# Kernel optimization log

Hardware: AMD Instinct MI355X
Metric: run time of the kernel (lower is better)

Reference implementation:

```python
import jax, jax.numpy as jnp
import numpy as np

N_HEAD = 16
N_EMBD = 1024
HEAD_DIM = N_EMBD // N_HEAD


def setup_inputs() -> dict:
    key = jax.random.key(0)
    k1, k2, k3 = jax.random.split(key, 3)
    B, T, C = 2, 2048, N_EMBD
    x = jax.random.normal(k1, (B, T, C), dtype=jnp.float32)
    # nn.Linear weights: (out_features, in_features)
    W_attn = jax.random.normal(k2, (3 * C, C), dtype=jnp.float32) * 0.02
    W_proj = jax.random.normal(k3, (C, C), dtype=jnp.float32) * 0.02
    return {"x": x, "W_attn": W_attn, "W_proj": W_proj}


def reference(x, W_attn, W_proj):
    B, T, C = x.shape
    h, hd = N_HEAD, HEAD_DIM
    # c_attn: x @ W^T, then split into q, k, v
    qkv = jnp.einsum('btc,dc->btd', x, W_attn)  # [B, T, 3C]
    q, k, v = jnp.split(qkv, 3, axis=-1)
    # [B, T, C] -> [B, h, T, hd]
    q = q.reshape(B, T, h, hd).transpose(0, 2, 1, 3)
    k = k.reshape(B, T, h, hd).transpose(0, 2, 1, 3)
    v = v.reshape(B, T, h, hd).transpose(0, 2, 1, 3)
    # NOTE: no 1/sqrt(hd) scaling in the original module
    logits = jnp.einsum('bhnk,bhmk->bhnm', q, k)  # [B, h, T, T]
    causal = jnp.tril(jnp.ones((T, T), dtype=bool))  # [T, T]
    logits = jnp.where(causal[None, None, :, :], logits, -jnp.inf)
    weights = jax.nn.softmax(logits, axis=-1)
    O = jnp.einsum('bhnm,bhmv->bhnv', weights, v)  # [B, h, T, hd]
    # Original: einsum('bhnv,hdv->bnd', O, c_proj.weight) with weight viewed as (h, d, v)
    Wp = W_proj.reshape(h, C, hd)
    Y = jnp.einsum('bhnv,hdv->bnd', O, Wp)  # [B, T, C]
    return Y
```

## Files before the change

kernel.cpp:

```cpp
#include <hip/hip_runtime.h>
#include <stdint.h>
#include <math.h>

#define B_    2
#define T_    2048
#define C_    1024
#define H_    16
#define D_    64
#define MTOT  4096
#define NQKV  3072
#define KDIM  1024

#define LOG2E 1.4426950408889634f

typedef short short8 __attribute__((ext_vector_type(8)));
typedef float f32x4  __attribute__((ext_vector_type(4)));

__device__ __forceinline__ uint16_t f2b(float f) {
    union { float f; uint32_t u; } x; x.f = f;
    uint32_t u = x.u;
    return (uint16_t)((u + 0x7FFFu + ((u >> 16) & 1u)) >> 16);
}
__device__ __forceinline__ uint32_t packb2(float a, float b) {
    union { float f; uint32_t u; } x, y; x.f = a; y.f = b;
    return ((x.u + 0x8000u) >> 16) | ((y.u + 0x8000u) & 0xffff0000u);
}
__device__ __forceinline__ uint32_t packb2_rne(float a, float b) {
    return (uint32_t)f2b(a) | ((uint32_t)f2b(b) << 16);
}
__device__ __forceinline__ float fexp2(float x) {
#if __has_builtin(__builtin_amdgcn_exp2f)
    return __builtin_amdgcn_exp2f(x);
#else
    return exp2f(x);
#endif
}

__global__ __launch_bounds__(256) void cast_all(const float* __restrict__ x,
                                                const float* __restrict__ wa,
                                                uint16_t* __restrict__ xb,
                                                uint16_t* __restrict__ wab,
                                                int n4x, int n4w) {
    int i = blockIdx.x * blockDim.x + threadIdx.x;
    const float* src; uint16_t* dst; int j;
    if (i < n4x) { src = x; dst = xb; j = i; }
    else { j = i - n4x; if (j >= n4w) return; src = wa; dst = wab; }
    float4 v = ((const float4*)src)[j];
    ushort4 o;
    o.x = f2b(v.x); o.y = f2b(v.y); o.z = f2b(v.z); o.w = f2b(v.w);
    ((ushort4*)dst)[j] = o;
}

__global__ __launch_bounds__(256) void cast_wp(const float* __restrict__ wp,
                                               uint16_t* __restrict__ wt) {
    int i = blockIdx.x * blockDim.x + threadIdx.x;
    int j4 = (i & 255) * 4;
    int d  = i >> 8;
    int h = j4 >> 6, v = j4 & 63;
    float4 val = *(const float4*)(wp + h * 65536 + d * 64 + v);
    ushort4 o;
    o.x = f2b(val.x); o.y = f2b(val.y); o.z = f2b(val.z); o.w = f2b(val.w);
    *(ushort4*)(wt + d * 1024 + j4) = o;
}

__global__ __launch_bounds__(256, 3) void gemm_qkv(const uint16_t* __restrict__ A,
                                                   const uint16_t* __restrict__ Bw,
                                                   uint16_t* __restrict__ qkvb) {
    __shared__ __align__(16) uint16_t As[128 * 64];
    __shared__ __align__(16) uint16_t Bs[128 * 64];

    int tid = threadIdx.x;
    int w = tid >> 6, lane = tid & 63;
    int qd = lane >> 4, ln = lane & 15;
    int lnx = ln & 7;
    int rowBase = blockIdx.y * 128;
    int colBase = blockIdx.x * 128;
    int mw = (w >> 1) * 64, nw = (w & 1) * 64;

    int srow = tid >> 3;
    int pchunk = tid & 7;
    int gchunk = pchunk ^ (srow & 7);

    const uint16_t* ga = A  + (size_t)(rowBase + srow) * KDIM + gchunk * 8;
    const uint16_t* gb = Bw + (size_t)(colBase + srow) * KDIM + gchunk * 8;
    uint16_t* la = &As[srow * 64 + pchunk * 8];
    uint16_t* lb = &Bs[srow * 64 + pchunk * 8];

    short8 pa[4], pb[4];
#pragma unroll
    for (int m = 0; m < 4; m++) {
        pa[m] = *(const short8*)(ga + (size_t)m * 32 * KDIM);
        pb[m] = *(const short8*)(gb + (size_t)m * 32 * KDIM);
    }

    f32x4 acc[4][4] = {};
    for (int s = 0; s < 16; s++) {
#pragma unroll
        for (int m = 0; m < 4; m++) {
            *(short8*)(la + m * 32 * 64) = pa[m];
            *(short8*)(lb + m * 32 * 64) = pb[m];
        }
        __syncthreads();
        if (s < 15) {
            int k0 = (s + 1) * 64;
#pragma unroll
            for (int m = 0; m < 4; m++) {
                pa[m] = *(const short8*)(ga + k0 + (size_t)m * 32 * KDIM);
                pb[m] = *(const short8*)(gb + k0 + (size_t)m * 32 * KDIM);
            }
        }
#pragma unroll
        for (int ks = 0; ks < 2; ks++) {
            int p = (ks * 4 + qd) ^ lnx;
            short8 a[4], b[4];
#pragma unroll
            for (int i = 0; i < 4; i++) {
                a[i] = *(const short8*)&As[(mw + i * 16 + ln) * 64 + p * 8];
                b[i] = *(const short8*)&Bs[(nw + i * 16 + ln) * 64 + p * 8];
            }
#pragma unroll
            for (int i = 0; i < 4; i++)
#pragma unroll
                for (int j = 0; j < 4; j++)
                    acc[i][j] = __builtin_amdgcn_mfma_f32_16x16x32_bf16(a[i], b[j], acc[i][j], 0, 0, 0);
        }
        __syncthreads();
    }

#pragma unroll
    for (int i = 0; i < 4; i++) {
#pragma unroll
        for (int j = 0; j < 4; j++) {
            int gcol = colBase + nw + j * 16 + ln;
            int which = gcol >> 10;
            int rem = gcol & 1023;
            int h = rem >> 6, d = rem & 63;
            float sc = (which == 0) ? LOG2E : 1.0f;
#pragma unroll
            for (int r = 0; r < 4; r++) {
                int grow = rowBase + mw + i * 16 + qd * 4 + r;
                int bb = grow >> 11, t = grow & 2047;
                uint16_t val = f2b(acc[i][j][r] * sc);
                if (which == 2) {
                    qkvb[(size_t)2 * 4194304 + (((size_t)(bb * H_ + h) * D_) + d) * T_ + t] = val;
                } else {
                    qkvb[(size_t)which * 4194304 + (((size_t)(bb * H_ + h) * T_) + t) * D_ + d] = val;
                }
            }
        }
    }
}

__global__ __launch_bounds__(128) void attn(const uint16_t* __restrict__ qkvb,
                                            uint16_t* __restrict__ oc) {
    union ShU {
        uint16_t Pl[2][64][72];
        struct { f32x4 Cb[16][64]; float Lb[64][4]; } c;
    };
    __shared__ __align__(16) ShU sh;

    int tid = threadIdx.x;
    int w = tid >> 6, lane = tid & 63;
    int qd = lane >> 4, ln = lane & 15;
    int bid = blockIdx.x;
    int qt = 31 - (bid >> 5);
    int bh = bid & 31;
    int qbase = qt * 64;
    int ntiles = qt + 1;

    const uint16_t* Q  = qkvb + (size_t)bh * T_ * D_;
    const uint16_t* K  = Q + 4194304;
    const uint16_t* Vt = qkvb + (size_t)2 * 4194304 + (size_t)bh * D_ * T_;

    short8 bq[4][2];
#pragma unroll
    for (int jq = 0; jq < 4; jq++)
#pragma unroll
        for (int ks = 0; ks < 2; ks++)
            bq[jq][ks] = *(const short8*)(Q + (size_t)(qbase + jq * 16 + ln) * D_ + ks * 32 + qd * 8);

    f32x4 ot[4][4] = {};
    float l_part[4] = {};

    for (int kt = w; kt < ntiles; kt += 2) {
        short8 ak[4][2], av[4][2];
#pragma unroll
        for (int it = 0; it < 4; it++)
#pragma unroll
            for (int ks = 0; ks < 2; ks++)
                ak[it][ks] = *(const short8*)(K + (size_t)(kt * 64 + it * 16 + ln) * D_ + ks * 32 + qd * 8);
#pragma unroll
        for (int id = 0; id < 4; id++)
#pragma unroll
            for (int ks = 0; ks < 2; ks++)
                av[id][ks] = *(const short8*)(Vt + (size_t)(id * 16 + ln) * T_ + kt * 64 + ks * 32 + qd * 8);

        bool diag = (kt == qt);
#pragma unroll
        for (int it = 0; it < 4; it++) {
            f32x4 stt[4] = {};
#pragma unroll
            for (int ks = 0; ks < 2; ks++)
#pragma unroll
                for (int jq = 0; jq < 4; jq++)
                    stt[jq] = __builtin_amdgcn_mfma_f32_16x16x32_bf16(ak[it][ks], bq[jq][ks], stt[jq], 0, 0, 0);
            if (diag) {
#pragma unroll
                for (int jq = 0; jq < 4; jq++)
#pragma unroll
                    for (int r = 0; r < 4; r++) {
                        int t = it * 16 + qd * 4 + r;
                        int q = jq * 16 + ln;
                        if (t > q) stt[jq][r] = -1.0e30f;
                    }
            }
#pragma unroll
            for (int jq = 0; jq < 4; jq++) {
                float p0 = fexp2(stt[jq][0]);
                float p1 = fexp2(stt[jq][1]);
                float p2 = fexp2(stt[jq][2]);
                float p3 = fexp2(stt[jq][3]);
                l_part[jq] += (p0 + p1) + (p2 + p3);
                uint2 pk;
                pk.x = packb2(p0, p1);
                pk.y = packb2(p2, p3);
                *(uint2*)&sh.Pl[w][jq * 16 + ln][it * 16 + qd * 4] = pk;
            }
        }

        short8 bp[4][2];
#pragma unroll
        for (int jq = 0; jq < 4; jq++)
#pragma unroll
            for (int ks = 0; ks < 2; ks++)
                bp[jq][ks] = *(const short8*)&sh.Pl[w][jq * 16 + ln][ks * 32 + qd * 8];

#pragma unroll
        for (int ks = 0; ks < 2; ks++)
#pragma unroll
            for (int id = 0; id < 4; id++)
#pragma unroll
                for (int jq = 0; jq < 4; jq++)
                    ot[id][jq] = __builtin_amdgcn_mfma_f32_16x16x32_bf16(av[id][ks], bp[jq][ks], ot[id][jq], 0, 0, 0);
    }

    __syncthreads();
    if (w == 1) {
#pragma unroll
        for (int id = 0; id < 4; id++)
#pragma unroll
            for (int jq = 0; jq < 4; jq++)
                sh.c.Cb[id * 4 + jq][lane] = ot[id][jq];
        f32x4 lp = { l_part[0], l_part[1], l_part[2], l_part[3] };
        *(f32x4*)&sh.c.Lb[lane][0] = lp;
    }
    __syncthreads();
    if (w == 0) {
#pragma unroll
        for (int id = 0; id < 4; id++)
#pragma unroll
            for (int jq = 0; jq < 4; jq++)
                ot[id][jq] += sh.c.Cb[id * 4 + jq][lane];
        f32x4 lo = *(const f32x4*)&sh.c.Lb[lane][0];
        float rl[4];
#pragma unroll
        for (int jq = 0; jq < 4; jq++) {
            float s = l_part[jq] + lo[jq];
            s += __shfl_xor(s, 16);
            s += __shfl_xor(s, 32);
            rl[jq] = 1.0f / s;
        }
        int b = bh >> 4, h = bh & 15;
#pragma unroll
        for (int id = 0; id < 4; id++)
#pragma unroll
            for (int jq = 0; jq < 4; jq++) {
                float v0 = ot[id][jq][0] * rl[jq];
                float v1 = ot[id][jq][1] * rl[jq];
                float v2 = ot[id][jq][2] * rl[jq];
                float v3 = ot[id][jq][3] * rl[jq];
                uint2 pk;
                pk.x = packb2_rne(v0, v1);
                pk.y = packb2_rne(v2, v3);
                int q = qbase + jq * 16 + ln;
                *(uint2*)&oc[(size_t)(b * T_ + q) * C_ + h * 64 + id * 16 + qd * 4] = pk;
            }
    }
}

__global__ __launch_bounds__(256, 3) void gemm_out(const uint16_t* __restrict__ A,
                                                   const uint16_t* __restrict__ Bw,
                                                   float* __restrict__ out) {
    __shared__ __align__(16) uint16_t As[128 * 64];
    __shared__ __align__(16) uint16_t Bs[64 * 64];

    int tid = threadIdx.x;
    int w = tid >> 6, lane = tid & 63;
    int qd = lane >> 4, ln = lane & 15;
    int lnx = ln & 7;
    int rowBase = blockIdx.y * 128;
    int colBase = blockIdx.x * 64;
    int mw = (w >> 1) * 64, nw = (w & 1) * 32;

    int srow = tid >> 3;
    int pchunk = tid & 7;
    int gchunk = pchunk ^ (srow & 7);

    const uint16_t* ga = A  + (size_t)(rowBase + srow) * KDIM + gchunk * 8;
    const uint16_t* gb = Bw + (size_t)(colBase + srow) * KDIM + gchunk * 8;
    uint16_t* la = &As[srow * 64 + pchunk * 8];
    uint16_t* lb = &Bs[srow * 64 + pchunk * 8];

    short8 pa[4], pb[2];
#pragma unroll
    for (int m = 0; m < 4; m++)
        pa[m] = *(const short8*)(ga + (size_t)m * 32 * KDIM);
#pragma unroll
    for (int m = 0; m < 2; m++)
        pb[m] = *(const short8*)(gb + (size_t)m * 32 * KDIM);

    f32x4 acc[4][2] = {};
    for (int s = 0; s < 16; s++) {
#pragma unroll
        for (int m = 0; m < 4; m++)
            *(short8*)(la + m * 32 * 64) = pa[m];
#pragma unroll
        for (int m = 0; m < 2; m++)
            *(short8*)(lb + m * 32 * 64) = pb[m];
        __syncthreads();
        if (s < 15) {
            int k0 = (s + 1) * 64;
#pragma unroll
            for (int m = 0; m < 4; m++)
                pa[m] = *(const short8*)(ga + k0 + (size_t)m * 32 * KDIM);
#pragma unroll
            for (int m = 0; m < 2; m++)
                pb[m] = *(const short8*)(gb + k0 + (size_t)m * 32 * KDIM);
        }
#pragma unroll
        for (int ks = 0; ks < 2; ks++) {
            int p = (ks * 4 + qd) ^ lnx;
            short8 a[4], b[2];
#pragma unroll
            for (int i = 0; i < 4; i++)
                a[i] = *(const short8*)&As[(mw + i * 16 + ln) * 64 + p * 8];
#pragma unroll
            for (int j = 0; j < 2; j++)
                b[j] = *(const short8*)&Bs[(nw + j * 16 + ln) * 64 + p * 8];
#pragma unroll
            for (int i = 0; i < 4; i++)
#pragma unroll
                for (int j = 0; j < 2; j++)
                    acc[i][j] = __builtin_amdgcn_mfma_f32_16x16x32_bf16(a[i], b[j], acc[i][j], 0, 0, 0);
        }
        __syncthreads();
    }

#pragma unroll
    for (int i = 0; i < 4; i++)
#pragma unroll
        for (int j = 0; j < 2; j++)
#pragma unroll
            for (int r = 0; r < 4; r++) {
                int grow = rowBase + mw + i * 16 + qd * 4 + r;
                int gcol = colBase + nw + j * 16 + ln;
                out[(size_t)grow * 1024 + gcol] = acc[i][j][r];
            }
}

extern "C" void kernel_launch(void* const* d_in, const int* in_sizes, int n_in,
                              void* d_out, int out_size, void* d_ws, size_t ws_size,
                              hipStream_t stream) {
    const float* x  = (const float*)d_in[0];
    const float* Wa = (const float*)d_in[1];
    const float* Wp = (const float*)d_in[2];
    float* out = (float*)d_out;

    uint16_t* ws   = (uint16_t*)d_ws;
    uint16_t* xb   = ws;
    uint16_t* Wab  = xb + 4194304;
    uint16_t* Wtb  = Wab + 3145728;
    uint16_t* qkvb = Wtb + 1048576;
    uint16_t* ob   = qkvb + (size_t)3 * 4194304;

    cast_all<<<7168, 256, 0, stream>>>(x, Wa, xb, Wab, 4194304 / 4, 3145728 / 4);
    cast_wp<<<1024, 256, 0, stream>>>(Wp, Wtb);
    gemm_qkv<<<dim3(24, 32), 256, 0, stream>>>(xb, Wab, qkvb);
    attn<<<1024, 128, 0, stream>>>(qkvb, ob);
    gemm_out<<<dim3(16, 32), 256, 0, stream>>>(ob, Wtb, out);
}
```

Baseline: 174.9 us.

## Split attention KV tiles across four waves and defer V loads

The attention kernel now uses four waves per block instead of two, with each wave striding over key tiles by four. The partial outputs and row sums are combined by a two-stage tree reduction through shared memory. V loads move to after the score/softmax phase to lower register pressure, and the P tile is read per k-slice. The bf16 pack also uses a single byte-permute instruction. This adds parallelism for the causal-attention blocks with long KV ranges, at the cost of more shared memory (padded P buffer), extra reduction barriers, and possibly lower occupancy.

```diff
diff --git a/kernel.cpp b/kernel.cpp
--- a/kernel.cpp
+++ b/kernel.cpp
@@ -23,7 +23,7 @@
 }
 __device__ __forceinline__ uint32_t packb2(float a, float b) {
     union { float f; uint32_t u; } x, y; x.f = a; y.f = b;
-    return ((x.u + 0x8000u) >> 16) | ((y.u + 0x8000u) & 0xffff0000u);
+    return __builtin_amdgcn_perm(y.u + 0x8000u, x.u + 0x8000u, 0x07060302u);
 }
 __device__ __forceinline__ uint32_t packb2_rne(float a, float b) {
     return (uint32_t)f2b(a) | ((uint32_t)f2b(b) << 16);
@@ -151,11 +151,11 @@
     }
 }
 
-__global__ __launch_bounds__(128) void attn(const uint16_t* __restrict__ qkvb,
-                                            uint16_t* __restrict__ oc) {
+__global__ __launch_bounds__(256, 3) void attn(const uint16_t* __restrict__ qkvb,
+                                               uint16_t* __restrict__ oc) {
     union ShU {
-        uint16_t Pl[2][64][72];
-        struct { f32x4 Cb[16][64]; float Lb[64][4]; } c;
+        uint16_t Pl[4][64][80];
+        f32x4 X[2][17][64];
     };
     __shared__ __align__(16) ShU sh;
 
@@ -182,18 +182,13 @@
     f32x4 ot[4][4] = {};
     float l_part[4] = {};
 
-    for (int kt = w; kt < ntiles; kt += 2) {
-        short8 ak[4][2], av[4][2];
+    for (int kt = w; kt < ntiles; kt += 4) {
+        short8 ak[4][2];
 #pragma unroll
         for (int it = 0; it < 4; it++)
 #pragma unroll
             for (int ks = 0; ks < 2; ks++)
                 ak[it][ks] = *(const short8*)(K + (size_t)(kt * 64 + it * 16 + ln) * D_ + ks * 32 + qd * 8);
-#pragma unroll
-        for (int id = 0; id < 4; id++)
-#pragma unroll
-            for (int ks = 0; ks < 2; ks++)
-                av[id][ks] = *(const short8*)(Vt + (size_t)(id * 16 + ln) * T_ + kt * 64 + ks * 32 + qd * 8);
 
         bool diag = (kt == qt);
 #pragma unroll
@@ -228,31 +223,54 @@
             }
         }
 
-        short8 bp[4][2];
-#pragma unroll
-        for (int jq = 0; jq < 4; jq++)
+        short8 av[4][2];
+#pragma unroll
+        for (int id = 0; id < 4; id++)
 #pragma unroll
             for (int ks = 0; ks < 2; ks++)
-                bp[jq][ks] = *(const short8*)&sh.Pl[w][jq * 16 + ln][ks * 32 + qd * 8];
-
-#pragma unroll
-        for (int ks = 0; ks < 2; ks++)
+                av[id][ks] = *(const short8*)(Vt + (size_t)(id * 16 + ln) * T_ + kt * 64 + ks * 32 + qd * 8);
+
+#pragma unroll
+        for (int ks = 0; ks < 2; ks++) {
+            short8 bp[4];
+#pragma unroll
+            for (int jq = 0; jq < 4; jq++)
+                bp[jq] = *(const short8*)&sh.Pl[w][jq * 16 + ln][ks * 32 + qd * 8];
 #pragma unroll
             for (int id = 0; id < 4; id++)
 #pragma unroll
                 for (int jq = 0; jq < 4; jq++)
-                    ot[id][jq] = __builtin_amdgcn_mfma_f32_16x16x32_bf16(av[id][ks], bp[jq][ks], ot[id][jq], 0, 0, 0);
-    }
-
+                    ot[id][jq] = __builtin_amdgcn_mfma_f32_16x16x32_bf16(av[id][ks], bp[jq], ot[id][jq], 0, 0, 0);
+        }
+    }
+
+    f32x4 lp = { l_part[0], l_part[1], l_part[2], l_part[3] };
+    __syncthreads();
+    if (w >= 2) {
+#pragma unroll
+        for (int id = 0; id < 4; id++)
+#pragma unroll
+            for (int jq = 0; jq < 4; jq++)
+                sh.X[w - 2][id * 4 + jq][lane] = ot[id][jq];
+        sh.X[w - 2][16][lane] = lp;
+    }
+    __syncthreads();
+    if (w < 2) {
+#pragma unroll
+        for (int id = 0; id < 4; id++)
+#pragma unroll
+            for (int jq = 0; jq < 4; jq++)
+                ot[id][jq] += sh.X[w][id * 4 + jq][lane];
+        lp += sh.X[w][16][lane];
+    }
     __syncthreads();
     if (w == 1) {
 #pragma unroll
         for (int id = 0; id < 4; id++)
 #pragma unroll
             for (int jq = 0; jq < 4; jq++)
-                sh.c.Cb[id * 4 + jq][lane] = ot[id][jq];
-        f32x4 lp = { l_part[0], l_part[1], l_part[2], l_part[3] };
-        *(f32x4*)&sh.c.Lb[lane][0] = lp;
+                sh.X[0][id * 4 + jq][lane] = ot[id][jq];
+        sh.X[0][16][lane] = lp;
     }
     __syncthreads();
     if (w == 0) {
@@ -260,12 +278,12 @@
         for (int id = 0; id < 4; id++)
 #pragma unroll
             for (int jq = 0; jq < 4; jq++)
-                ot[id][jq] += sh.c.Cb[id * 4 + jq][lane];
-        f32x4 lo = *(const f32x4*)&sh.c.Lb[lane][0];
+                ot[id][jq] += sh.X[0][id * 4 + jq][lane];
+        lp += sh.X[0][16][lane];
         float rl[4];
 #pragma unroll
         for (int jq = 0; jq < 4; jq++) {
-            float s = l_part[jq] + lo[jq];
+            float s = lp[jq];
             s += __shfl_xor(s, 16);
             s += __shfl_xor(s, 32);
             rl[jq] = 1.0f / s;
@@ -386,6 +404,6 @@
     cast_all<<<7168, 256, 0, stream>>>(x, Wa, xb, Wab, 4194304 / 4, 3145728 / 4);
     cast_wp<<<1024, 256, 0, stream>>>(Wp, Wtb);
     gemm_qkv<<<dim3(24, 32), 256, 0, stream>>>(xb, Wab, qkvb);
-    attn<<<1024, 128, 0, stream>>>(qkvb, ob);
+    attn<<<1024, 256, 0, stream>>>(qkvb, ob);
     gemm_out<<<dim3(16, 32), 256, 0, stream>>>(ob, Wtb, out);
 }
```

Measured after the change: 232.4 us. 32.9% more time.
